# Optimization experiments

Measured on AMD Instinct MI355X. Metric: run time of the kernel, lower is better.

The kernel has to match this reference:

```python
import jax, jax.numpy as jnp
import numpy as np

B, T, D = 2, 2048, 4096
H, HKV, HD = 32, 8, 128
N_REP = H // HKV
THETA = 500000.0


def _rope(x, cos, sin):
    # x: [B, T, h, HD]; cos/sin: [T, HD//2]
    xr = x.reshape(*x.shape[:-1], HD // 2, 2)
    x0, x1 = xr[..., 0], xr[..., 1]
    c = cos[None, :, None, :]
    s = sin[None, :, None, :]
    o0 = x0 * c - x1 * s
    o1 = x0 * s + x1 * c
    return jnp.stack([o0, o1], axis=-1).reshape(x.shape)


def setup_inputs() -> dict:
    key = jax.random.key(0)
    ks = jax.random.split(key, 8)
    x = jax.random.normal(ks[0], (B, T, D), dtype=jnp.float32)
    # true Llama RoPE angles
    inv_freq = 1.0 / (THETA ** (np.arange(0, HD, 2, dtype=np.float32) / HD))
    ang = np.outer(np.arange(T, dtype=np.float32), inv_freq)  # [T, HD//2]
    freqs_cos = jnp.asarray(np.cos(ang), dtype=jnp.float32)
    freqs_sin = jnp.asarray(np.sin(ang), dtype=jnp.float32)
    mask = jnp.zeros((T, T), dtype=jnp.float32)  # accepted but unused (as in source)
    cache_k = jnp.zeros((B, T, HKV, HD), dtype=jnp.float32)
    cache_v = jnp.zeros((B, T, HKV, HD), dtype=jnp.float32)
    sc = 0.02
    wq = jax.random.normal(ks[1], (D, H * HD), dtype=jnp.float32) * sc
    wk = jax.random.normal(ks[2], (D, HKV * HD), dtype=jnp.float32) * sc
    wv = jax.random.normal(ks[3], (D, HKV * HD), dtype=jnp.float32) * sc
    wo = jax.random.normal(ks[4], (H * HD, D), dtype=jnp.float32) * sc
    return {"x": x, "freqs_cos": freqs_cos, "freqs_sin": freqs_sin, "mask": mask,
            "cache_k": cache_k, "cache_v": cache_v,
            "wq": wq, "wk": wk, "wv": wv, "wo": wo, "start_pos": 0}


def reference(x, freqs_cos, freqs_sin, mask, cache_k, cache_v, wq, wk, wv, wo, start_pos):
    b, t, _ = x.shape
    q = (x @ wq).reshape(b, t, H, HD)
    k = (x @ wk).reshape(b, t, HKV, HD)
    v = (x @ wv).reshape(b, t, HKV, HD)
    q = _rope(q, freqs_cos, freqs_sin)
    k = _rope(k, freqs_cos, freqs_sin)
    # KV-cache write
    cache_k = jax.lax.dynamic_update_slice(cache_k, k, (0, start_pos, 0, 0))
    cache_v = jax.lax.dynamic_update_slice(cache_v, v, (0, start_pos, 0, 0))
    s_len = start_pos + t
    keys = jnp.repeat(cache_k[:, :s_len], N_REP, axis=2)    # [B, S, H, HD]
    values = jnp.repeat(cache_v[:, :s_len], N_REP, axis=2)  # [B, S, H, HD]
    # per-head scaled dot-product attention (vectorized over heads)
    scores = jnp.einsum('bthd,bshd->bhts', q, keys) / jnp.sqrt(jnp.float32(HD))
    probs = jax.nn.softmax(scores, axis=-1)  # mask is NOT applied in the source forward
    out = jnp.einsum('bhts,bshd->bthd', probs, values).reshape(b, t, H * HD)
    return out @ wo
```

## Files before the change

### kernel.cpp

```cpp
#include <hip/hip_runtime.h>

typedef unsigned short u16;
typedef unsigned int   u32;
typedef __attribute__((ext_vector_type(2))) unsigned int u32x2;
typedef __attribute__((ext_vector_type(4))) float f32x4;
typedef __attribute__((ext_vector_type(8))) short s16x8;
typedef __attribute__((ext_vector_type(4))) _Float16 f16x4;
typedef __attribute__((ext_vector_type(8))) _Float16 f16x8;

#define B_   2
#define T_   2048
#define D_   4096
#define H_   32
#define HKV_ 8
#define HD_  128
#define NQKV 6144
#define M_   (B_*T_)

__device__ __forceinline__ u16 f2bf(float f){
  u32 u = __float_as_uint(f);
  u += 0x7fffu + ((u >> 16) & 1u);
  return (u16)(u >> 16);
}
__device__ __forceinline__ float bf2f(u16 h){
  return __uint_as_float(((u32)h) << 16);
}
__device__ __forceinline__ void gload16(const void* g, void* l){
  __builtin_amdgcn_global_load_lds(
      (const __attribute__((address_space(1))) u32*)g,
      (__attribute__((address_space(3))) u32*)l, 16, 0, 0);
}

__global__ void k_convert_x(const float* __restrict__ in, u16* __restrict__ out){
  int i = blockIdx.x * 256 + threadIdx.x;
  float4 v = reinterpret_cast<const float4*>(in)[i];
  u32 lo = (u32)f2bf(v.x) | ((u32)f2bf(v.y) << 16);
  u32 hi = (u32)f2bf(v.z) | ((u32)f2bf(v.w) << 16);
  u32x2 p; p.x = lo; p.y = hi;
  reinterpret_cast<u32x2*>(out)[i] = p;
}

__global__ void k_transpose_w(const float* __restrict__ in, u16* __restrict__ out,
                              int K, int N){
  __shared__ float tile[64][65];
  int n0 = blockIdx.x * 64, k0 = blockIdx.y * 64;
  int tid = threadIdx.x;
  int tx = tid & 15, ty = tid >> 4;
  #pragma unroll
  for (int rr = 0; rr < 4; rr++) {
    int r = ty + 16 * rr;
    float4 v = *reinterpret_cast<const float4*>(in + (size_t)(k0 + r) * N + n0 + 4 * tx);
    tile[r][4 * tx + 0] = v.x; tile[r][4 * tx + 1] = v.y;
    tile[r][4 * tx + 2] = v.z; tile[r][4 * tx + 3] = v.w;
  }
  __syncthreads();
  #pragma unroll
  for (int ni = 0; ni < 4; ni++) {
    int nn = ty + 16 * ni;
    ushort4 o;
    o.x = f2bf(tile[4 * tx + 0][nn]);
    o.y = f2bf(tile[4 * tx + 1][nn]);
    o.z = f2bf(tile[4 * tx + 2][nn]);
    o.w = f2bf(tile[4 * tx + 3][nn]);
    *reinterpret_cast<ushort4*>(out + (size_t)(n0 + nn) * K + k0 + 4 * tx) = o;
  }
}

template<int OUT_F32>
__global__ __launch_bounds__(256, 2) void k_gemm(
    const u16* __restrict__ A, const u16* __restrict__ Bt,
    void* __restrict__ Cv, int M, int N, int K)
{
  __shared__ __attribute__((aligned(16))) unsigned char smem[32768];
  unsigned char* As = smem;
  unsigned char* Bs = smem + 16384;
  const int tid = threadIdx.x;
  const int w = tid >> 6, l = tid & 63;
  const int m0 = blockIdx.y * 128, n0 = blockIdx.x * 128;
  const int wm = (w >> 1) * 64, wn = (w & 1) * 64;
  f32x4 acc[4][4];
  #pragma unroll
  for (int i = 0; i < 4; i++)
    #pragma unroll
    for (int j = 0; j < 4; j++)
      acc[i][j] = f32x4{0.f, 0.f, 0.f, 0.f};

  const int srcoff = 8 * ((l & 7) ^ ((l >> 3) & 7));
  const int subrow = l >> 3;

  for (int k0 = 0; k0 < K; k0 += 64) {
    if (k0) __syncthreads();
    #pragma unroll
    for (int i = 0; i < 4; i++) {
      int chunk = 4 * w + i;
      int row = chunk * 8 + subrow;
      gload16(A  + (size_t)(m0 + row) * K + k0 + srcoff, As + chunk * 1024);
      gload16(Bt + (size_t)(n0 + row) * K + k0 + srcoff, Bs + chunk * 1024);
    }
    asm volatile("s_waitcnt vmcnt(0)" ::: "memory");
    __syncthreads();
    #pragma unroll
    for (int kk = 0; kk < 2; kk++) {
      s16x8 a[4], b[4];
      const int co = kk * 64 + 16 * (l >> 4);
      #pragma unroll
      for (int mi = 0; mi < 4; mi++) {
        int r = wm + 16 * mi + (l & 15);
        a[mi] = *reinterpret_cast<const s16x8*>(As + r * 128 + (co ^ ((r & 7) << 4)));
      }
      #pragma unroll
      for (int ni = 0; ni < 4; ni++) {
        int r = wn + 16 * ni + (l & 15);
        b[ni] = *reinterpret_cast<const s16x8*>(Bs + r * 128 + (co ^ ((r & 7) << 4)));
      }
      #pragma unroll
      for (int mi = 0; mi < 4; mi++)
        #pragma unroll
        for (int ni = 0; ni < 4; ni++)
          acc[mi][ni] = __builtin_amdgcn_mfma_f32_16x16x32_bf16(a[mi], b[ni], acc[mi][ni], 0, 0, 0);
    }
  }
  const int g = l >> 4, c = l & 15;
  #pragma unroll
  for (int mi = 0; mi < 4; mi++)
    #pragma unroll
    for (int ni = 0; ni < 4; ni++)
      #pragma unroll
      for (int r = 0; r < 4; r++) {
        int m = m0 + wm + 16 * mi + 4 * g + r;
        int n = n0 + wn + 16 * ni + c;
        float v = acc[mi][ni][r];
        if (OUT_F32) reinterpret_cast<float*>(Cv)[(size_t)m * N + n] = v;
        else         reinterpret_cast<u16*>(Cv)[(size_t)m * N + n] = f2bf(v);
      }
}

#define BARX  asm volatile("s_barrier" ::: "memory")
#define PRIO1 __builtin_amdgcn_s_setprio(1)
#define PRIO0 __builtin_amdgcn_s_setprio(0)
#define VM4   asm volatile("s_waitcnt vmcnt(4)" ::: "memory")
#define VM0   asm volatile("s_waitcnt vmcnt(0)" ::: "memory")
#define LGKM0 do { asm volatile("s_waitcnt lgkmcnt(0)" ::: "memory"); \
                   __builtin_amdgcn_sched_barrier(0); } while (0)

#define AS_(b) (smem + (b) * 65536)
#define BS_(b) (smem + (b) * 65536 + 32768)
#define STAGE_HA(buf, half, kt) { \
  _Pragma("unroll") for (int r2 = 0; r2 < 2; r2++) { \
    int rw = (half) * 128 + r2 * 64 + w * 8; \
    gload16(A + (size_t)(m0 + rw + subrow) * K + (kt) * 64 + srcoff, \
            AS_(buf) + rw * 128); } }
#define STAGE_HB(buf, half, kt) { \
  _Pragma("unroll") for (int r2 = 0; r2 < 2; r2++) { \
    int rw = (half) * 128 + r2 * 64 + w * 8; \
    gload16(Bt + (size_t)(n0 + rw + subrow) * K + (kt) * 64 + srcoff, \
            BS_(buf) + rw * 128); } }
#define RD_A2(buf, p) { \
  _Pragma("unroll") for (int rt = 0; rt < 2; rt++) { \
    int row = wr * 128 + (p) * 32 + rt * 16 + c; \
    const unsigned char* ptr = AS_(buf) + row * 128; \
    int sw = (row & 7) << 4; \
    af[rt][0] = *(const s16x8*)(ptr + ((16 * g) ^ sw)); \
    af[rt][1] = *(const s16x8*)(ptr + ((64 + 16 * g) ^ sw)); } }
#define RD_B8(buf) { \
  _Pragma("unroll") for (int ni = 0; ni < 4; ni++) { \
    int row = wc * 64 + ni * 16 + c; \
    const unsigned char* ptr = BS_(buf) + row * 128; \
    int sw = (row & 7) << 4; \
    bfr[ni][0] = *(const s16x8*)(ptr + ((16 * g) ^ sw)); \
    bfr[ni][1] = *(const s16x8*)(ptr + ((64 + 16 * g) ^ sw)); } }
#define MFP(p) { \
  _Pragma("unroll") for (int rt = 0; rt < 2; rt++) \
  _Pragma("unroll") for (int ni = 0; ni < 4; ni++) \
  _Pragma("unroll") for (int kk = 0; kk < 2; kk++) \
    acc[(p) * 2 + rt][ni] = __builtin_amdgcn_mfma_f32_16x16x32_bf16( \
        af[rt][kk], bfr[ni][kk], acc[(p) * 2 + rt][ni], 0, 0, 0); }

__global__ __launch_bounds__(512, 1) void k_gemm8(
    const u16* __restrict__ A, const u16* __restrict__ Bt,
    float* __restrict__ Cv, int M, int N, int K)
{
  __shared__ __attribute__((aligned(16))) unsigned char smem[131072];
  const int tid = threadIdx.x;
  const int w = tid >> 6, l = tid & 63;
  const int c = l & 15, g = l >> 4;
  const int wr = w >> 2, wc = w & 3;

  const int nbx = N >> 8;
  const int nwg = nbx * (M >> 8);
  const int orig = blockIdx.x;
  const int id = (orig & 7) * (nwg >> 3) + (orig >> 3);
  const int m0 = (id / nbx) << 8;
  const int n0 = (id % nbx) << 8;

  const int srcoff = 8 * ((l & 7) ^ ((l >> 3) & 7));
  const int subrow = l >> 3;

  f32x4 acc[8][4];
  #pragma unroll
  for (int i = 0; i < 8; i++)
    #pragma unroll
    for (int j = 0; j < 4; j++)
      acc[i][j] = f32x4{0.f, 0.f, 0.f, 0.f};
  s16x8 af[2][2], bfr[4][2];

  STAGE_HB(0, 0, 0); STAGE_HB(0, 1, 0);
  STAGE_HA(0, 0, 0); STAGE_HA(0, 1, 0);
  STAGE_HB(1, 0, 1); STAGE_HB(1, 1, 1);
  VM4; BARX;

  const int NT2 = K >> 7;
  for (int it = 0; it < NT2; ++it) {
    const int tA = 2 * it, tB = 2 * it + 1;
    const bool st = (it < NT2 - 1);
    RD_A2(0, 0); RD_B8(0); STAGE_HA(1, 0, tB);
    BARX; LGKM0; PRIO1; MFP(0); PRIO0; BARX;
    RD_A2(0, 1); STAGE_HA(1, 1, tB);
    BARX; LGKM0; PRIO1; MFP(1); PRIO0; BARX;
    RD_A2(0, 2); if (st) STAGE_HB(0, 0, tA + 2);
    BARX; LGKM0; PRIO1; MFP(2); PRIO0; BARX;
    RD_A2(0, 3); if (st) STAGE_HB(0, 1, tA + 2);
    BARX; LGKM0; PRIO1; MFP(3); PRIO0;
    if (st) { VM4; } else { VM0; }
    BARX;
    RD_A2(1, 0); RD_B8(1); if (st) STAGE_HA(0, 0, tA + 2);
    BARX; LGKM0; PRIO1; MFP(0); PRIO0; BARX;
    RD_A2(1, 1); if (st) STAGE_HA(0, 1, tA + 2);
    BARX; LGKM0; PRIO1; MFP(1); PRIO0; BARX;
    RD_A2(1, 2); if (st) STAGE_HB(1, 0, tB + 2);
    BARX; LGKM0; PRIO1; MFP(2); PRIO0; BARX;
    RD_A2(1, 3); if (st) STAGE_HB(1, 1, tB + 2);
    BARX; LGKM0; PRIO1; MFP(3); PRIO0;
    if (st) { VM4; }
    BARX;
  }

  #pragma unroll
  for (int mi = 0; mi < 8; mi++)
    #pragma unroll
    for (int ni = 0; ni < 4; ni++)
      #pragma unroll
      for (int r = 0; r < 4; r++) {
        int m = m0 + wr * 128 + 16 * mi + 4 * g + r;
        int n = n0 + wc * 64 + 16 * ni + c;
        Cv[(size_t)m * N + n] = acc[mi][ni][r];
      }
}

__global__ void k_rope_q(u16* C1, const float* __restrict__ fc, const float* __restrict__ fs){
  int idx = blockIdx.x * 256 + threadIdx.x;
  int m = idx >> 11, p = idx & 2047;
  int h = p >> 6, i = p & 63;
  int t = m & (T_ - 1);
  u32* ptr = reinterpret_cast<u32*>(C1 + (size_t)m * NQKV + h * HD_ + 2 * i);
  u32 u = *ptr;
  float x0 = __uint_as_float(u << 16);
  float x1 = __uint_as_float(u & 0xffff0000u);
  float cc = fc[t * 64 + i], ss = fs[t * 64 + i];
  float o0 = x0 * cc - x1 * ss;
  float o1 = x0 * ss + x1 * cc;
  *ptr = (u32)f2bf(o0) | ((u32)f2bf(o1) << 16);
}

__global__ void k_rope_k(const u16* __restrict__ C1, const float* __restrict__ fc,
                         const float* __restrict__ fs, unsigned char* __restrict__ Kg){
  int idx = blockIdx.x * 256 + threadIdx.x;
  int m = idx >> 9, p = idx & 511;
  int kh = p >> 6, i = p & 63;
  int b = m >> 11, t = m & (T_ - 1);
  u32 u = *reinterpret_cast<const u32*>(C1 + (size_t)m * NQKV + D_ + kh * HD_ + 2 * i);
  float x0 = __uint_as_float(u << 16);
  float x1 = __uint_as_float(u & 0xffff0000u);
  float cc = fc[t * 64 + i], ss = fs[t * 64 + i];
  float o0 = x0 * cc - x1 * ss;
  float o1 = x0 * ss + x1 * cc;
  u32 packed = (u32)f2bf(o0) | ((u32)f2bf(o1) << 16);
  unsigned char* Kbb = Kg + (size_t)(b * HKV_ + kh) * 524288;
  int swb = (((i >> 2) ^ (t & 7)) << 4) | (4 * (i & 3));
  *reinterpret_cast<u32*>(Kbb + (size_t)t * 256 + swb) = packed;
}

__global__ void k_v_trans(const u16* __restrict__ C1, unsigned char* __restrict__ Vg){
  __shared__ float tile[32][33];
  int bz = blockIdx.z;
  int t0 = blockIdx.x * 32, d0 = blockIdx.y * 32;
  int tx = threadIdx.x, ty = threadIdx.y;
  int b = bz >> 3, kh = bz & 7;
  const u16* src = C1 + (size_t)(b * T_) * NQKV + D_ + HKV_ * HD_ + kh * HD_;
  #pragma unroll
  for (int i = ty; i < 32; i += 8)
    tile[i][tx] = bf2f(src[(size_t)(t0 + i) * NQKV + d0 + tx]);
  __syncthreads();
  unsigned char* Vbb = Vg + (size_t)bz * 524288;
  #pragma unroll
  for (int i = ty; i < 32; i += 8) {
    int d = d0 + i;
    int k = t0 + tx;
    int tt = k >> 6, kv = k & 63;
    int pp = (kv & 0x23) | ((kv & 0x10) >> 2) | ((kv & 0x0C) << 1);
    int swb = (((pp >> 3) ^ (d & 7)) << 4) | (2 * (pp & 7));
    *reinterpret_cast<_Float16*>(Vbb + (size_t)tt * 16384 + d * 128 + swb) =
        (_Float16)tile[tx][i];
  }
}

__global__ __launch_bounds__(256, 2) void k_attn(
    const u16* __restrict__ Q,
    const unsigned char* __restrict__ Kg,
    const unsigned char* __restrict__ Vg,
    u16* __restrict__ Ob)
{
  __shared__ __attribute__((aligned(16))) unsigned char smem[49152];
  const int tid = threadIdx.x;
  const int w = tid >> 6, l = tid & 63;
  const int c = l & 15, g = l >> 4;
  const int q0 = blockIdx.x * 128 + w * 32;
  const int h = blockIdx.y, b = blockIdx.z;
  const int kh = h >> 2;
  const unsigned char* Kb_ = Kg + (size_t)(b * HKV_ + kh) * 524288;
  const unsigned char* Vb_ = Vg + (size_t)(b * HKV_ + kh) * 524288;

  const float SCL2 = 0.08838834764831845f * 1.4426950408889634f;
  const float OFF2 = 14.4269504f;

  s16x8 qf[2][4];
  #pragma unroll
  for (int qt = 0; qt < 2; qt++)
    #pragma unroll
    for (int ci = 0; ci < 4; ci++)
      qf[qt][ci] = *reinterpret_cast<const s16x8*>(
          Q + (size_t)(b * T_ + q0 + 16 * qt + c) * NQKV + h * HD_ + 32 * ci + 8 * g);

  f32x4 o[2][8];
  #pragma unroll
  for (int qt = 0; qt < 2; qt++)
    #pragma unroll
    for (int i = 0; i < 8; i++) o[qt][i] = f32x4{0.f, 0.f, 0.f, 0.f};
  float lsum[2] = {0.f, 0.f};

  auto stageK = [&](int bi, int tt) {
    const unsigned char* Ks = Kb_ + (size_t)tt * 16384;
    unsigned char* Kl = smem + bi * 16384;
    #pragma unroll
    for (int i = 0; i < 4; i++) {
      int ch = i * 4 + w;
      gload16(Ks + ch * 1024 + l * 16, Kl + ch * 1024);
    }
  };
  auto stageV = [&](int tt) {
    const unsigned char* Vs = Vb_ + (size_t)tt * 16384;
    unsigned char* Vl = smem + 32768;
    #pragma unroll
    for (int i = 0; i < 4; i++) {
      int ch = i * 4 + w;
      gload16(Vs + ch * 1024 + l * 16, Vl + ch * 1024);
    }
  };

  stageK(0, 0);
  asm volatile("s_waitcnt vmcnt(0)" ::: "memory");
  __syncthreads();

  for (int tt = 0; tt < T_ / 64; ++tt) {
    int cur = tt & 1;
    stageV(tt);
    if (tt < T_ / 64 - 1) stageK(cur ^ 1, tt + 1);
    const unsigned char* Kl = smem + cur * 16384;
    const unsigned char* Vl = smem + 32768;

    f32x4 s[4][2];
    #pragma unroll
    for (int mi = 0; mi < 4; mi++)
      #pragma unroll
      for (int qt = 0; qt < 2; qt++) s[mi][qt] = f32x4{0.f, 0.f, 0.f, 0.f};

    #pragma unroll
    for (int mi = 0; mi < 4; mi++) {
      const int row = 16 * mi + c;
      const int sw = (row & 7) << 4;
      s16x8 kf[4];
      #pragma unroll
      for (int ci = 0; ci < 4; ci++)
        kf[ci] = *reinterpret_cast<const s16x8*>(Kl + row * 256 + ((64 * ci + 16 * g) ^ sw));
      #pragma unroll
      for (int qt = 0; qt < 2; qt++)
        #pragma unroll
        for (int ci = 0; ci < 4; ci++)
          s[mi][qt] = __builtin_amdgcn_mfma_f32_16x16x32_bf16(kf[ci], qf[qt][ci], s[mi][qt], 0, 0, 0);
    }

    f16x8 pa8[2][2];
    #pragma unroll
    for (int qt = 0; qt < 2; qt++)
      #pragma unroll
      for (int mi = 0; mi < 4; mi++)
        #pragma unroll
        for (int r = 0; r < 4; r++) {
          float p = exp2f(s[mi][qt][r] * SCL2 - OFF2);
          lsum[qt] += p;
          pa8[qt][mi >> 1][(mi & 1) * 4 + r] = (_Float16)p;
        }

    if (tt < T_ / 64 - 1) asm volatile("s_waitcnt vmcnt(4)" ::: "memory");
    else                  asm volatile("s_waitcnt vmcnt(0)" ::: "memory");
    __syncthreads();

    #pragma unroll
    for (int cp = 0; cp < 2; cp++)
      #pragma unroll
      for (int dc = 0; dc < 8; dc++) {
        const int d = 16 * dc + c;
        f16x8 v8 = *reinterpret_cast<const f16x8*>(
            Vl + d * 128 + ((64 * cp + 16 * g) ^ ((d & 7) << 4)));
        #pragma unroll
        for (int qt = 0; qt < 2; qt++)
          o[qt][dc] = __builtin_amdgcn_mfma_f32_16x16x32_f16(pa8[qt][cp], v8, o[qt][dc], 0, 0, 0);
      }

    asm volatile("s_waitcnt vmcnt(0)" ::: "memory");
    __syncthreads();
  }

  #pragma unroll
  for (int qt = 0; qt < 2; qt++) {
    lsum[qt] += __shfl_xor(lsum[qt], 16);
    lsum[qt] += __shfl_xor(lsum[qt], 32);
  }
  float inv[2][4];
  #pragma unroll
  for (int qt = 0; qt < 2; qt++)
    #pragma unroll
    for (int r = 0; r < 4; r++)
      inv[qt][r] = 1.0f / __shfl(lsum[qt], 4 * g + r, 64);

  #pragma unroll
  for (int qt = 0; qt < 2; qt++) {
    u16* Orow = Ob + (size_t)(b * T_ + q0 + 16 * qt) * D_ + h * HD_;
    #pragma unroll
    for (int dc = 0; dc < 8; dc++)
      #pragma unroll
      for (int r = 0; r < 4; r++)
        Orow[(size_t)(4 * g + r) * D_ + 16 * dc + c] = f2bf(o[qt][dc][r] * inv[qt][r]);
  }
}

extern "C" void kernel_launch(void* const* d_in, const int* in_sizes, int n_in,
                              void* d_out, int out_size, void* d_ws, size_t ws_size,
                              hipStream_t stream)
{
  const float* x  = (const float*)d_in[0];
  const float* fc = (const float*)d_in[1];
  const float* fs = (const float*)d_in[2];
  const float* wq = (const float*)d_in[6];
  const float* wk = (const float*)d_in[7];
  const float* wv = (const float*)d_in[8];
  const float* wo = (const float*)d_in[9];

  unsigned char* w = (unsigned char*)d_ws;
  u16* Xb   = (u16*)(w);
  u16* Wt   = (u16*)(w + 33554432ull);
  u16* Wot  = (u16*)(w + 83886080ull);
  u16* C1   = (u16*)(w + 117440512ull);
  unsigned char* Kg = w + 167772160ull;
  unsigned char* Vg = w + 176160768ull;
  u16* Ob   = (u16*)(w + 184549376ull);

  k_convert_x<<<16384, 256, 0, stream>>>(x, Xb);
  k_transpose_w<<<dim3(64, 64), 256, 0, stream>>>(wq, Wt, D_, D_);
  k_transpose_w<<<dim3(16, 64), 256, 0, stream>>>(wk, Wt + (size_t)D_ * D_, D_, 1024);
  k_transpose_w<<<dim3(16, 64), 256, 0, stream>>>(wv, Wt + (size_t)5120 * D_, D_, 1024);
  k_transpose_w<<<dim3(64, 64), 256, 0, stream>>>(wo, Wot, D_, D_);

  k_gemm<0><<<dim3(NQKV / 128, M_ / 128), 256, 0, stream>>>(Xb, Wt, C1, M_, NQKV, D_);

  k_rope_q<<<32768, 256, 0, stream>>>(C1, fc, fs);
  k_rope_k<<<8192, 256, 0, stream>>>(C1, fc, fs, Kg);
  k_v_trans<<<dim3(64, 4, 16), dim3(32, 8), 0, stream>>>(C1, Vg);

  k_attn<<<dim3(T_ / 128, H_, B_), 256, 0, stream>>>(C1, Kg, Vg, Ob);

  k_gemm8<<<(D_ / 256) * (M_ / 256), 512, 0, stream>>>(Ob, Wot, (float*)d_out, M_, D_, D_);
}
```

Baseline: 565.2 us.

## Replace QKV projection GEMM with 8-wave 256x192 pipelined tile kernel

Adds a new 512-thread GEMM kernel for the QKV projection. It uses a 256x192 output tile, double-buffered LDS staging with interleaved async global loads, a swizzled layout, priority-raised MFMA phases and a remapped block ordering. Only 512 workgroups are launched, about one per CU wave slot, replacing the previous 128x128 tile GEMM with 1536 blocks. The aim is more data reuse per tile and better load/compute overlap, at the cost of heavy register use and a single-block-per-CU occupancy.

```diff
diff --git a/kernel.cpp b/kernel.cpp
--- a/kernel.cpp
+++ b/kernel.cpp
@@ -139,9 +139,112 @@
 #define PRIO1 __builtin_amdgcn_s_setprio(1)
 #define PRIO0 __builtin_amdgcn_s_setprio(0)
 #define VM4   asm volatile("s_waitcnt vmcnt(4)" ::: "memory")
+#define VM3   asm volatile("s_waitcnt vmcnt(3)" ::: "memory")
 #define VM0   asm volatile("s_waitcnt vmcnt(0)" ::: "memory")
 #define LGKM0 do { asm volatile("s_waitcnt lgkmcnt(0)" ::: "memory"); \
                    __builtin_amdgcn_sched_barrier(0); } while (0)
+
+#define QAS_(b) (smem + (b) * 57344)
+#define QBS_(b) (smem + (b) * 57344 + 32768)
+#define Q_AU(buf, u, kt) { \
+    int rw = (u) * 64 + w * 8; \
+    gload16(A + (size_t)(m0 + rw + subrow) * K + (kt) * 64 + srcoff, \
+            QAS_(buf) + rw * 128); }
+#define Q_BU(buf, u, kt) { \
+    int rw = (u) * 64 + w * 8; \
+    gload16(Bt + (size_t)(n0 + rw + subrow) * K + (kt) * 64 + srcoff, \
+            QBS_(buf) + rw * 128); }
+#define Q_RD_A2(buf, p) { \
+  _Pragma("unroll") for (int rt = 0; rt < 2; rt++) { \
+    int row = wr * 128 + (p) * 32 + rt * 16 + c; \
+    const unsigned char* ptr = QAS_(buf) + row * 128; \
+    int sw = (row & 7) << 4; \
+    af[rt][0] = *(const s16x8*)(ptr + ((16 * g) ^ sw)); \
+    af[rt][1] = *(const s16x8*)(ptr + ((64 + 16 * g) ^ sw)); } }
+#define Q_RD_B6(buf) { \
+  _Pragma("unroll") for (int ni = 0; ni < 3; ni++) { \
+    int row = wc * 48 + ni * 16 + c; \
+    const unsigned char* ptr = QBS_(buf) + row * 128; \
+    int sw = (row & 7) << 4; \
+    bfr[ni][0] = *(const s16x8*)(ptr + ((16 * g) ^ sw)); \
+    bfr[ni][1] = *(const s16x8*)(ptr + ((64 + 16 * g) ^ sw)); } }
+#define Q_MFP(p) { \
+  _Pragma("unroll") for (int rt = 0; rt < 2; rt++) \
+  _Pragma("unroll") for (int ni = 0; ni < 3; ni++) \
+  _Pragma("unroll") for (int kk = 0; kk < 2; kk++) \
+    acc[(p) * 2 + rt][ni] = __builtin_amdgcn_mfma_f32_16x16x32_bf16( \
+        af[rt][kk], bfr[ni][kk], acc[(p) * 2 + rt][ni], 0, 0, 0); }
+
+__global__ __launch_bounds__(512, 1) void k_gemm8q(
+    const u16* __restrict__ A, const u16* __restrict__ Bt,
+    u16* __restrict__ Cv, int M, int N, int K)
+{
+  __shared__ __attribute__((aligned(16))) unsigned char smem[114688];
+  const int tid = threadIdx.x;
+  const int w = tid >> 6, l = tid & 63;
+  const int c = l & 15, g = l >> 4;
+  const int wr = w >> 2, wc = w & 3;
+
+  const int nbx = N / 192;
+  const int nwg = nbx * (M >> 8);
+  const int orig = blockIdx.x;
+  const int id = (orig & 7) * (nwg >> 3) + (orig >> 3);
+  const int m0 = (id / nbx) << 8;
+  const int n0 = (id % nbx) * 192;
+
+  const int srcoff = 8 * ((l & 7) ^ ((l >> 3) & 7));
+  const int subrow = l >> 3;
+
+  f32x4 acc[8][3];
+  #pragma unroll
+  for (int i = 0; i < 8; i++)
+    #pragma unroll
+    for (int j = 0; j < 3; j++)
+      acc[i][j] = f32x4{0.f, 0.f, 0.f, 0.f};
+  s16x8 af[2][2], bfr[3][2];
+
+  Q_BU(0, 0, 0); Q_BU(0, 1, 0); Q_BU(0, 2, 0);
+  Q_AU(0, 0, 0); Q_AU(0, 1, 0); Q_AU(0, 2, 0); Q_AU(0, 3, 0);
+  Q_BU(1, 0, 1); Q_BU(1, 1, 1); Q_BU(1, 2, 1);
+  VM3; BARX;
+
+  const int NT2 = K >> 7;
+  for (int it = 0; it < NT2; ++it) {
+    const int tA = 2 * it, tB = 2 * it + 1;
+    const bool st = (it < NT2 - 1);
+    Q_RD_A2(0, 0); Q_RD_B6(0); Q_AU(1, 0, tB); Q_AU(1, 1, tB);
+    BARX; LGKM0; PRIO1; Q_MFP(0); PRIO0; BARX;
+    Q_RD_A2(0, 1); Q_AU(1, 2, tB); Q_AU(1, 3, tB);
+    BARX; LGKM0; PRIO1; Q_MFP(1); PRIO0; BARX;
+    Q_RD_A2(0, 2); if (st) { Q_BU(0, 0, tA + 2); Q_BU(0, 1, tA + 2); }
+    BARX; LGKM0; PRIO1; Q_MFP(2); PRIO0; BARX;
+    Q_RD_A2(0, 3); if (st) Q_BU(0, 2, tA + 2);
+    BARX; LGKM0; PRIO1; Q_MFP(3); PRIO0;
+    if (st) { VM3; } else { VM0; }
+    BARX;
+    Q_RD_A2(1, 0); Q_RD_B6(1); if (st) { Q_AU(0, 0, tA + 2); Q_AU(0, 1, tA + 2); }
+    BARX; LGKM0; PRIO1; Q_MFP(0); PRIO0; BARX;
+    Q_RD_A2(1, 1); if (st) { Q_AU(0, 2, tA + 2); Q_AU(0, 3, tA + 2); }
+    BARX; LGKM0; PRIO1; Q_MFP(1); PRIO0; BARX;
+    Q_RD_A2(1, 2); if (st) { Q_BU(1, 0, tB + 2); Q_BU(1, 1, tB + 2); }
+    BARX; LGKM0; PRIO1; Q_MFP(2); PRIO0; BARX;
+    Q_RD_A2(1, 3); if (st) Q_BU(1, 2, tB + 2);
+    BARX; LGKM0; PRIO1; Q_MFP(3); PRIO0;
+    if (st) { VM3; }
+    BARX;
+  }
+
+  #pragma unroll
+  for (int mi = 0; mi < 8; mi++)
+    #pragma unroll
+    for (int ni = 0; ni < 3; ni++)
+      #pragma unroll
+      for (int r = 0; r < 4; r++) {
+        int m = m0 + wr * 128 + 16 * mi + 4 * g + r;
+        int n = n0 + wc * 48 + 16 * ni + c;
+        Cv[(size_t)m * N + n] = f2bf(acc[mi][ni][r]);
+      }
+}
 
 #define AS_(b) (smem + (b) * 65536)
 #define BS_(b) (smem + (b) * 65536 + 32768)
@@ -471,7 +574,7 @@
   k_transpose_w<<<dim3(16, 64), 256, 0, stream>>>(wv, Wt + (size_t)5120 * D_, D_, 1024);
   k_transpose_w<<<dim3(64, 64), 256, 0, stream>>>(wo, Wot, D_, D_);
 
-  k_gemm<0><<<dim3(NQKV / 128, M_ / 128), 256, 0, stream>>>(Xb, Wt, C1, M_, NQKV, D_);
+  k_gemm8q<<<512, 512, 0, stream>>>(Xb, Wt, C1, M_, NQKV, D_);
 
   k_rope_q<<<32768, 256, 0, stream>>>(C1, fc, fs);
   k_rope_k<<<8192, 256, 0, stream>>>(C1, fc, fs, Kg);
```

New measurement: 547.0 us. 1.03x faster.

## Route Q projection through 256-tile GEMM and fuse prep and RoPE launches

Applied to the files above, without the earlier changes.

The fused QKV projection is split in two. The Q part (N=4096) now runs on the larger 256x256 pipelined k_gemm8 kernel writing bf16 with a leading dimension, and the K/V part (N=2048) stays on the 128-tile GEMM. The x conversion and four weight transposes are merged into one k_prep launch, and the Q and K RoPE kernels into one k_rope launch, to cut launch overhead and tail gaps. The prep grid gives the narrow wk/wv slices 64 x-blocks each, most of which exit early, and adding a second GEMM launch adds a serial step.

```diff
diff --git a/kernel.cpp b/kernel.cpp
--- a/kernel.cpp
+++ b/kernel.cpp
@@ -31,21 +31,35 @@
       (__attribute__((address_space(3))) u32*)l, 16, 0, 0);
 }
 
-__global__ void k_convert_x(const float* __restrict__ in, u16* __restrict__ out){
-  int i = blockIdx.x * 256 + threadIdx.x;
-  float4 v = reinterpret_cast<const float4*>(in)[i];
-  u32 lo = (u32)f2bf(v.x) | ((u32)f2bf(v.y) << 16);
-  u32 hi = (u32)f2bf(v.z) | ((u32)f2bf(v.w) << 16);
-  u32x2 p; p.x = lo; p.y = hi;
-  reinterpret_cast<u32x2*>(out)[i] = p;
-}
-
-__global__ void k_transpose_w(const float* __restrict__ in, u16* __restrict__ out,
-                              int K, int N){
+__global__ void k_prep(const float* __restrict__ x,
+                       const float* __restrict__ wq, const float* __restrict__ wk,
+                       const float* __restrict__ wv, const float* __restrict__ wo,
+                       u16* __restrict__ Xb, u16* __restrict__ Wt,
+                       u16* __restrict__ Wot){
   __shared__ float tile[64][65];
-  int n0 = blockIdx.x * 64, k0 = blockIdx.y * 64;
-  int tid = threadIdx.x;
-  int tx = tid & 15, ty = tid >> 4;
+  const int z = blockIdx.z;
+  const int tid = threadIdx.x;
+  if (z == 4) {
+    size_t base = ((size_t)blockIdx.y * 64 + blockIdx.x) * 1024 + tid;
+    #pragma unroll
+    for (int r = 0; r < 4; r++) {
+      size_t i = base + r * 256;
+      float4 v = reinterpret_cast<const float4*>(x)[i];
+      u32 lo = (u32)f2bf(v.x) | ((u32)f2bf(v.y) << 16);
+      u32 hi = (u32)f2bf(v.z) | ((u32)f2bf(v.w) << 16);
+      u32x2 p; p.x = lo; p.y = hi;
+      reinterpret_cast<u32x2*>(Xb)[i] = p;
+    }
+    return;
+  }
+  const float* in; u16* out; int N;
+  if      (z == 0) { in = wq; out = Wt;                        N = 4096; }
+  else if (z == 1) { in = wk; out = Wt + (size_t)D_ * D_;      N = 1024; }
+  else if (z == 2) { in = wv; out = Wt + (size_t)5120 * D_;    N = 1024; }
+  else             { in = wo; out = Wot;                       N = 4096; }
+  const int n0 = blockIdx.x * 64, k0 = blockIdx.y * 64;
+  if (n0 >= N) return;
+  const int tx = tid & 15, ty = tid >> 4;
   #pragma unroll
   for (int rr = 0; rr < 4; rr++) {
     int r = ty + 16 * rr;
@@ -62,14 +76,14 @@
     o.y = f2bf(tile[4 * tx + 1][nn]);
     o.z = f2bf(tile[4 * tx + 2][nn]);
     o.w = f2bf(tile[4 * tx + 3][nn]);
-    *reinterpret_cast<ushort4*>(out + (size_t)(n0 + nn) * K + k0 + 4 * tx) = o;
+    *reinterpret_cast<ushort4*>(out + (size_t)(n0 + nn) * D_ + k0 + 4 * tx) = o;
   }
 }
 
 template<int OUT_F32>
 __global__ __launch_bounds__(256, 2) void k_gemm(
     const u16* __restrict__ A, const u16* __restrict__ Bt,
-    void* __restrict__ Cv, int M, int N, int K)
+    void* __restrict__ Cv, int M, int N, int K, int ldc)
 {
   __shared__ __attribute__((aligned(16))) unsigned char smem[32768];
   unsigned char* As = smem;
@@ -130,8 +144,8 @@
         int m = m0 + wm + 16 * mi + 4 * g + r;
         int n = n0 + wn + 16 * ni + c;
         float v = acc[mi][ni][r];
-        if (OUT_F32) reinterpret_cast<float*>(Cv)[(size_t)m * N + n] = v;
-        else         reinterpret_cast<u16*>(Cv)[(size_t)m * N + n] = f2bf(v);
+        if (OUT_F32) reinterpret_cast<float*>(Cv)[(size_t)m * ldc + n] = v;
+        else         reinterpret_cast<u16*>(Cv)[(size_t)m * ldc + n] = f2bf(v);
       }
 }
 
@@ -176,9 +190,10 @@
     acc[(p) * 2 + rt][ni] = __builtin_amdgcn_mfma_f32_16x16x32_bf16( \
         af[rt][kk], bfr[ni][kk], acc[(p) * 2 + rt][ni], 0, 0, 0); }
 
+template<int OUT_F32>
 __global__ __launch_bounds__(512, 1) void k_gemm8(
     const u16* __restrict__ A, const u16* __restrict__ Bt,
-    float* __restrict__ Cv, int M, int N, int K)
+    void* __restrict__ Cv, int M, int N, int K, int ldc)
 {
   __shared__ __attribute__((aligned(16))) unsigned char smem[131072];
   const int tid = threadIdx.x;
@@ -243,41 +258,44 @@
       for (int r = 0; r < 4; r++) {
         int m = m0 + wr * 128 + 16 * mi + 4 * g + r;
         int n = n0 + wc * 64 + 16 * ni + c;
-        Cv[(size_t)m * N + n] = acc[mi][ni][r];
+        float v = acc[mi][ni][r];
+        if (OUT_F32) reinterpret_cast<float*>(Cv)[(size_t)m * ldc + n] = v;
+        else         reinterpret_cast<u16*>(Cv)[(size_t)m * ldc + n] = f2bf(v);
       }
 }
 
-__global__ void k_rope_q(u16* C1, const float* __restrict__ fc, const float* __restrict__ fs){
-  int idx = blockIdx.x * 256 + threadIdx.x;
-  int m = idx >> 11, p = idx & 2047;
-  int h = p >> 6, i = p & 63;
-  int t = m & (T_ - 1);
-  u32* ptr = reinterpret_cast<u32*>(C1 + (size_t)m * NQKV + h * HD_ + 2 * i);
-  u32 u = *ptr;
-  float x0 = __uint_as_float(u << 16);
-  float x1 = __uint_as_float(u & 0xffff0000u);
-  float cc = fc[t * 64 + i], ss = fs[t * 64 + i];
-  float o0 = x0 * cc - x1 * ss;
-  float o1 = x0 * ss + x1 * cc;
-  *ptr = (u32)f2bf(o0) | ((u32)f2bf(o1) << 16);
-}
-
-__global__ void k_rope_k(const u16* __restrict__ C1, const float* __restrict__ fc,
-                         const float* __restrict__ fs, unsigned char* __restrict__ Kg){
-  int idx = blockIdx.x * 256 + threadIdx.x;
-  int m = idx >> 9, p = idx & 511;
-  int kh = p >> 6, i = p & 63;
-  int b = m >> 11, t = m & (T_ - 1);
-  u32 u = *reinterpret_cast<const u32*>(C1 + (size_t)m * NQKV + D_ + kh * HD_ + 2 * i);
-  float x0 = __uint_as_float(u << 16);
-  float x1 = __uint_as_float(u & 0xffff0000u);
-  float cc = fc[t * 64 + i], ss = fs[t * 64 + i];
-  float o0 = x0 * cc - x1 * ss;
-  float o1 = x0 * ss + x1 * cc;
-  u32 packed = (u32)f2bf(o0) | ((u32)f2bf(o1) << 16);
-  unsigned char* Kbb = Kg + (size_t)(b * HKV_ + kh) * 524288;
-  int swb = (((i >> 2) ^ (t & 7)) << 4) | (4 * (i & 3));
-  *reinterpret_cast<u32*>(Kbb + (size_t)t * 256 + swb) = packed;
+__global__ void k_rope(u16* __restrict__ C1, const float* __restrict__ fc,
+                       const float* __restrict__ fs, unsigned char* __restrict__ Kg){
+  const int bid = blockIdx.x;
+  if (bid < 32768) {
+    int idx = bid * 256 + threadIdx.x;
+    int m = idx >> 11, p = idx & 2047;
+    int h = p >> 6, i = p & 63;
+    int t = m & (T_ - 1);
+    u32* ptr = reinterpret_cast<u32*>(C1 + (size_t)m * NQKV + h * HD_ + 2 * i);
+    u32 u = *ptr;
+    float x0 = __uint_as_float(u << 16);
+    float x1 = __uint_as_float(u & 0xffff0000u);
+    float cc = fc[t * 64 + i], ss = fs[t * 64 + i];
+    float o0 = x0 * cc - x1 * ss;
+    float o1 = x0 * ss + x1 * cc;
+    *ptr = (u32)f2bf(o0) | ((u32)f2bf(o1) << 16);
+  } else {
+    int idx = (bid - 32768) * 256 + threadIdx.x;
+    int m = idx >> 9, p = idx & 511;
+    int kh = p >> 6, i = p & 63;
+    int b = m >> 11, t = m & (T_ - 1);
+    u32 u = *reinterpret_cast<const u32*>(C1 + (size_t)m * NQKV + D_ + kh * HD_ + 2 * i);
+    float x0 = __uint_as_float(u << 16);
+    float x1 = __uint_as_float(u & 0xffff0000u);
+    float cc = fc[t * 64 + i], ss = fs[t * 64 + i];
+    float o0 = x0 * cc - x1 * ss;
+    float o1 = x0 * ss + x1 * cc;
+    u32 packed = (u32)f2bf(o0) | ((u32)f2bf(o1) << 16);
+    unsigned char* Kbb = Kg + (size_t)(b * HKV_ + kh) * 524288;
+    int swb = (((i >> 2) ^ (t & 7)) << 4) | (4 * (i & 3));
+    *reinterpret_cast<u32*>(Kbb + (size_t)t * 256 + swb) = packed;
+  }
 }
 
 __global__ void k_v_trans(const u16* __restrict__ C1, unsigned char* __restrict__ Vg){
@@ -465,19 +483,16 @@
   unsigned char* Vg = w + 176160768ull;
   u16* Ob   = (u16*)(w + 184549376ull);
 
-  k_convert_x<<<16384, 256, 0, stream>>>(x, Xb);
-  k_transpose_w<<<dim3(64, 64), 256, 0, stream>>>(wq, Wt, D_, D_);
-  k_transpose_w<<<dim3(16, 64), 256, 0, stream>>>(wk, Wt + (size_t)D_ * D_, D_, 1024);
-  k_transpose_w<<<dim3(16, 64), 256, 0, stream>>>(wv, Wt + (size_t)5120 * D_, D_, 1024);
-  k_transpose_w<<<dim3(64, 64), 256, 0, stream>>>(wo, Wot, D_, D_);
-
-  k_gemm<0><<<dim3(NQKV / 128, M_ / 128), 256, 0, stream>>>(Xb, Wt, C1, M_, NQKV, D_);
-
-  k_rope_q<<<32768, 256, 0, stream>>>(C1, fc, fs);
-  k_rope_k<<<8192, 256, 0, stream>>>(C1, fc, fs, Kg);
+  k_prep<<<dim3(64, 64, 5), 256, 0, stream>>>(x, wq, wk, wv, wo, Xb, Wt, Wot);
+
+  k_gemm8<0><<<(D_ / 256) * (M_ / 256), 512, 0, stream>>>(Xb, Wt, C1, M_, D_, D_, NQKV);
+  k_gemm<0><<<dim3(2048 / 128, M_ / 128), 256, 0, stream>>>(
+      Xb, Wt + (size_t)D_ * D_, C1 + D_, M_, 2048, D_, NQKV);
+
+  k_rope<<<40960, 256, 0, stream>>>(C1, fc, fs, Kg);
   k_v_trans<<<dim3(64, 4, 16), dim3(32, 8), 0, stream>>>(C1, Vg);
 
   k_attn<<<dim3(T_ / 128, H_, B_), 256, 0, stream>>>(C1, Kg, Vg, Ob);
 
-  k_gemm8<<<(D_ / 256) * (M_ / 256), 512, 0, stream>>>(Ob, Wot, (float*)d_out, M_, D_, D_);
-}
+  k_gemm8<1><<<(D_ / 256) * (M_ / 256), 512, 0, stream>>>(Ob, Wot, d_out, M_, D_, D_, D_);
+}
```

New measurement: 550.9 us. 1.03x faster.
